# Performance work log

Measured on AMD Instinct MI355X. Metric: run time of the kernel, lower is better.

## Reference

```python
import jax, jax.numpy as jnp
import numpy as np
import heapq
from collections import defaultdict

N_PER, N_BATCH, C = 100000, 2, 128  # nodes per graph, num graphs, feature dim
TARGET = 50000                      # target node count per graph


def _build_graph():
    # Symmetric degree-4 ring graph per batch (offsets +/-1, +/-2), required so
    # neighbours[] lookups in the collapse algorithm never miss.
    within = np.tile(np.arange(N_PER), N_BATCH)
    base = np.repeat(np.arange(N_BATCH) * N_PER, N_PER)
    src_all, dst_all = [], []
    for o in (1, 2, -1, -2):
        src_all.append(base + within)
        dst_all.append(base + (within + o) % N_PER)
    ei = np.stack([np.concatenate(src_all), np.concatenate(dst_all)]).astype(np.int64)
    batch = np.repeat(np.arange(N_BATCH), N_PER).astype(np.int64)
    return ei, batch


def _collapse(x, edge_index, target_edge_count, batch):
    # Faithful port of the sequential heap-driven greedy collapse.
    N = x.shape[0]
    collapse_mask = np.ones(N, dtype=bool)
    x_mask = np.ones(N, dtype=bool)
    neighbours = defaultdict(list)
    for f, t in zip(edge_index[0].tolist(), edge_index[1].tolist()):
        neighbours[f].append(t)
    for batch_id in range(int(batch.max()) + 1):
        node_ids = np.nonzero(batch == batch_id)[0]
        num_nodes = int(node_ids.shape[0])
        mags = (x[node_ids] * x[node_ids]).sum(axis=1)  # squared magnitude priority
        heap = [[float(m), int(n)] for m, n in zip(mags, node_ids)]
        heapq.heapify(heap)
        while num_nodes > target_edge_count:
            if len(heap) == 0:
                break
            _, node_id = heapq.heappop(heap)
            node_id = int(node_id)
            if not collapse_mask[node_id]:
                continue
            collapse_mask[node_id] = False
            neighbour_ids = neighbours[node_id]
            num_nodes -= 1
            new_neighbour_ids = []
            for nb in neighbour_ids:
                x_mask[nb] = False
                collapse_mask[nb] = False
                num_nodes -= 1
                for nbnb in neighbours[nb]:
                    if nbnb in neighbour_ids or nbnb == node_id:
                        continue
                    new_neighbour_ids.append(nbnb)
                    neighbours[nbnb] = [n for n in neighbours[nbnb] if n != nb]
                    neighbours[nbnb].append(node_id)
            neighbours[node_id] = new_neighbour_ids
    # Remap surviving nodes to compact ids and rebuild edge_index.
    old_to_new = -np.ones(N, dtype=np.int64)
    new_to_old = np.nonzero(x_mask)[0]
    old_to_new[new_to_old] = np.arange(new_to_old.shape[0])
    rows, cols = [], []
    for new_id, old_id in enumerate(new_to_old.tolist()):
        for nid in neighbours[old_id]:
            rows.append(new_id)
            cols.append(int(old_to_new[nid]))
    new_ei = np.array([rows, cols], dtype=np.int64)
    return x_mask, new_ei


def setup_inputs() -> dict:
    key = jax.random.key(0)
    ei, batch = _build_graph()
    x = jax.random.normal(key, (N_BATCH * N_PER, C), dtype=jnp.float32)
    return {
        "x": x,
        "edge_index": jnp.asarray(ei),
        "target_edge_count": TARGET,
        "batch": jnp.asarray(batch),
        "vertices": jnp.zeros((1,), dtype=jnp.int32),
        "edges": jnp.zeros((1,), dtype=jnp.int32),
    }


def reference(x, edge_index, target_edge_count, batch, vertices, edges):
    # vertices/edges are unused by the original forward.
    x_mask, new_ei = _collapse(
        np.asarray(x), np.asarray(edge_index), int(target_edge_count), np.asarray(batch)
    )
    keep = jnp.asarray(np.nonzero(x_mask)[0])
    return x[keep], jnp.asarray(new_ei), batch[keep]
```

## Files before the change

kernel.cpp:

```cpp
#include <hip/hip_runtime.h>
#include <stdint.h>

#define N_PER   100000
#define N_TOT   200000
#define C_DIM   128
#define PAD     131072
#define NBLK    782
#define CMW     ((N_PER + 31) / 32)
#define MAXL    512

typedef unsigned long long u64;

#define WAIT_LDS() asm volatile("s_waitcnt lgkmcnt(0)" ::: "memory")
#define WAIT_ALL() asm volatile("s_waitcnt vmcnt(0) lgkmcnt(0)" ::: "memory")

__device__ __forceinline__ float mag128(const float4* __restrict__ p4) {
  float4 u = p4[0], v = p4[1];
  float r0 = __fmul_rn(u.x,u.x), r1 = __fmul_rn(u.y,u.y),
        r2 = __fmul_rn(u.z,u.z), r3 = __fmul_rn(u.w,u.w),
        r4 = __fmul_rn(v.x,v.x), r5 = __fmul_rn(v.y,v.y),
        r6 = __fmul_rn(v.z,v.z), r7 = __fmul_rn(v.w,v.w);
  #pragma unroll
  for (int m = 1; m < 16; ++m) {
    u = p4[2*m]; v = p4[2*m+1];
    r0 = __fadd_rn(r0, __fmul_rn(u.x,u.x));
    r1 = __fadd_rn(r1, __fmul_rn(u.y,u.y));
    r2 = __fadd_rn(r2, __fmul_rn(u.z,u.z));
    r3 = __fadd_rn(r3, __fmul_rn(u.w,u.w));
    r4 = __fadd_rn(r4, __fmul_rn(v.x,v.x));
    r5 = __fadd_rn(r5, __fmul_rn(v.y,v.y));
    r6 = __fadd_rn(r6, __fmul_rn(v.z,v.z));
    r7 = __fadd_rn(r7, __fmul_rn(v.w,v.w));
  }
  return __fadd_rn(__fadd_rn(__fadd_rn(r0,r1), __fadd_rn(r2,r3)),
                   __fadd_rn(__fadd_rn(r4,r5), __fadd_rn(r6,r7)));
}

__global__ void k_init_keys(const float* __restrict__ x, u64* __restrict__ keys) {
  int slot = blockIdx.x*blockDim.x + threadIdx.x;
  if (slot >= 2*PAD) return;
  int b = slot >> 17;
  int w = slot & (PAD-1);
  if (w < N_PER) {
    int node = b*N_PER + w;
    float mag = mag128((const float4*)(x + (size_t)node*C_DIM));
    keys[slot] = ((u64)__float_as_uint(mag) << 32) | (uint32_t)node;
  } else {
    keys[slot] = ~0ull;
  }
}

__global__ void k_init_graph(int* __restrict__ nbr, uint8_t* __restrict__ xm, int cap) {
  int node = blockIdx.x*blockDim.x + threadIdx.x;
  if (node >= N_TOT) return;
  int base = (node >= N_PER) ? N_PER : 0;
  int w = node - base;
  int* Lp = nbr + (size_t)node*cap;
  Lp[0] = 4;
  Lp[1] = base + (w + 1) % N_PER;
  Lp[2] = base + (w + 2) % N_PER;
  Lp[3] = base + (w + N_PER - 1) % N_PER;
  Lp[4] = base + (w + N_PER - 2) % N_PER;
  xm[node] = 1;
}

__global__ void k_bitonic(u64* __restrict__ keys, int k, int j) {
  int i = blockIdx.x*blockDim.x + threadIdx.x;
  if (i >= 2*PAD) return;
  int ixj = i ^ j;
  if (ixj <= i) return;
  int wi = i & (PAD-1);
  bool asc = ((wi & k) == 0);
  u64 a = keys[i], b = keys[ixj];
  bool sw = asc ? (a > b) : (a < b);
  if (sw) { keys[i] = b; keys[ixj] = a; }
}

__global__ __launch_bounds__(64) void k_collapse(const u64* __restrict__ keys,
                                                 int* __restrict__ nbr,
                                                 uint8_t* __restrict__ xm,
                                                 const int* __restrict__ tgt_p,
                                                 int cap) {
  __shared__ uint32_t s_cm[CMW];
  __shared__ uint32_t s_mm[CMW];
  __shared__ uint32_t s_dirty[CMW];
  __shared__ int      s_prow[MAXL];
  __shared__ int      s_mem[4][MAXL];
  __shared__ int      s_memlen[4];
  __shared__ int      s_cand[MAXL];

  const int b    = blockIdx.x;
  const int lane = threadIdx.x;
  const int TGT  = tgt_p[0];
  const u64* ord = keys + (size_t)b * PAD;
  const int gbase = b * N_PER;

  for (int w = lane; w < CMW; w += 64) { s_cm[w]=0xffffffffu; s_mm[w]=0u; s_dirty[w]=0u; }
  WAIT_LDS();

  int num_nodes = N_PER;
  int  pfnode = -1;
  bool pfbad  = true;
  int4 pfreg  = make_int4(0,0,0,0);

  auto drain = [&]() {
    WAIT_ALL();
    for (int w = lane; w < CMW; w += 64) s_dirty[w] = 0u;
    pfbad = true;
    WAIT_LDS();
  };

  for (int base2 = 0; base2 < N_PER && num_nodes > TGT; base2 += 64) {
    int nd_l = (base2 + lane < N_PER) ? (int)(uint32_t)ord[base2 + lane] : -1;
    bool alive = false;
    if (base2 + lane < N_PER) {
      int ll = nd_l - gbase;
      alive = ((s_cm[ll>>5] >> (ll&31)) & 1u) != 0u;
    }
    u64 mask = __ballot(alive);
    while (mask != 0ull && num_nodes > TGT) {
      int k2 = __ffsll((long long)mask) - 1;
      mask &= mask - 1ull;
      int node = __shfl(nd_l, k2);
      int local = node - gbase;
      if (((s_cm[local>>5] >> (local&31)) & 1u) == 0u) continue;

      bool ndirty = ((s_dirty[local>>5] >> (local&31)) & 1u) != 0u;
      bool usepf = (node == pfnode) && !pfbad && !ndirty;
      int4 rv = make_int4(0,0,0,0);
      if (usepf) {
        if (lane < 16) rv = pfreg;
      } else {
        if (ndirty) drain();
        if (lane < 16) rv = *(const int4*)(nbr + (size_t)node*cap + 4*lane);
      }
      int L = __shfl(rv.x, 0);
      if (lane < 16) {
        int bs = 4*lane;
        if (lane == 0) { s_prow[0]=rv.y; s_prow[1]=rv.z; s_prow[2]=rv.w; }
        else { s_prow[bs-1]=rv.x; s_prow[bs]=rv.y; s_prow[bs+1]=rv.z; s_prow[bs+2]=rv.w; }
      }
      if (L > 62) {
        for (int i = 63 + lane; i < L; i += 64) s_prow[i] = nbr[(size_t)node*cap + 1 + i];
      }
      WAIT_LDS();

      if (lane == 0) atomicAnd(&s_cm[local>>5], ~(1u << (local&31)));
      for (int i = lane; i < L; i += 64) {
        int mv = s_prow[i];
        xm[mv] = 0;
        int ml = mv - gbase;
        atomicAnd(&s_cm[ml>>5], ~(1u << (ml&31)));
        atomicOr (&s_mm[ml>>5],  1u << (ml&31));
      }
      num_nodes -= 1 + L;
      WAIT_LDS();

      {
        u64 nm = mask;
        int npf = -1;
        while (nm != 0ull) {
          int kk = __ffsll((long long)nm) - 1;
          int cnd = __shfl(nd_l, kk);
          int cl = cnd - gbase;
          if (((s_cm[cl>>5] >> (cl&31)) & 1u) != 0u) { npf = cnd; break; }
          nm &= nm - 1ull;
        }
        pfnode = npf;
        pfbad = true;
        if (npf >= 0) {
          int pl = npf - gbase;
          bool pd = ((s_dirty[pl>>5] >> (pl&31)) & 1u) != 0u;
          if (!pd) {
            pfbad = false;
            if (lane < 16) pfreg = *(const int4*)(nbr + (size_t)npf*cap + 4*lane);
          }
        }
      }

      {
        bool md = false;
        for (int i = lane; i < L; i += 64) {
          int ml = s_prow[i] - gbase;
          md |= ((s_dirty[ml>>5] >> (ml&31)) & 1u) != 0u;
        }
        if (__ballot(md) != 0ull) drain();
      }

      int Ctot = 0;
      for (int mc = 0; mc < L; mc += 4) {
        int Lc = (L - mc < 4) ? (L - mc) : 4;
        int m0 = s_prow[mc];
        int m1 = (Lc > 1) ? s_prow[mc+1] : -1;
        int m2 = (Lc > 2) ? s_prow[mc+2] : -1;
        int m3 = (Lc > 3) ? s_prow[mc+3] : -1;

        int g = lane >> 4, jj = lane & 15;
        const int* tlg = nullptr;
        if (g < Lc) {
          int m = (g==0)?m0:(g==1)?m1:(g==2)?m2:m3;
          tlg = nbr + (size_t)m * cap;
          int4 c0 = *(const int4*)(tlg + 4*jj);
          if (jj == 0) s_memlen[g] = c0.x;
          else         s_mem[g][4*jj-1] = c0.x;
          s_mem[g][4*jj+0] = c0.y;
          s_mem[g][4*jj+1] = c0.z;
          s_mem[g][4*jj+2] = c0.w;
        }
        WAIT_LDS();
        if (g < Lc) {
          int lg = s_memlen[g];
          for (int s0 = 64 + 4*jj; s0 <= lg; s0 += 64) {
            int4 cv = *(const int4*)(tlg + s0);
            s_mem[g][s0-1] = cv.x;
            if (s0+1 <= lg) s_mem[g][s0+0] = cv.y;
            if (s0+2 <= lg) s_mem[g][s0+1] = cv.z;
            if (s0+3 <= lg) s_mem[g][s0+2] = cv.w;
          }
        }
        WAIT_LDS();

        int len0=(Lc>0)?s_memlen[0]:0, len1=(Lc>1)?s_memlen[1]:0,
            len2=(Lc>2)?s_memlen[2]:0, len3=(Lc>3)?s_memlen[3]:0;
        int o1=len0, o2=o1+len1, o3=o2+len2, T=o3+len3;

        for (int cb = 0; cb < T; cb += 64) {
          int i = cb + lane;
          bool act = i < T;
          int val = -1, gg = 0;
          if (act) {
            gg = (i>=o1) + (i>=o2) + (i>=o3);
            int qb = (gg==0)?0:(gg==1)?o1:(gg==2)?o2:o3;
            val = s_mem[gg][i-qb];
          }
          bool ism = !act || (val == node);
          if (act && !ism) {
            int vl = val - gbase;
            ism |= ((s_mm[vl>>5] >> (vl&31)) & 1u) != 0u;
          }
          bool keep = act && !ism;
          u64 mk = __ballot(keep);
          int wcnt = __popcll(mk);
          if (keep) {
            int pos = Ctot + __popcll(mk & ((1ull<<lane)-1ull));
            if (pos < cap - 1) s_cand[pos] = val;
          }
          if (wcnt) {
            bool td = false;
            if (keep) {
              int vl = val - gbase;
              td = ((s_dirty[vl>>5] >> (vl&31)) & 1u) != 0u;
            }
            if (__ballot(td) != 0ull) drain();

            int Twin = (T - cb < 64) ? (T - cb) : 64;
            uint32_t pk = keep ? (((uint32_t)val << 2) | (uint32_t)gg) : 0xffffffffu;
            bool owner = keep;
            uint32_t rmg = 0;
            int kocc = 0;
            for (int q = 0; q < Twin; ++q) {
              uint32_t pq = __shfl(pk, q);
              if (pq != 0xffffffffu && keep && (int)(pq >> 2) == val) {
                rmg |= 1u << (pq & 3u);
                ++kocc;
                if (q < lane) owner = false;
              }
            }
            if (owner) {
              bool u0=(rmg&1u)!=0, u1=(rmg&2u)!=0, u2=(rmg&4u)!=0, u3=(rmg&8u)!=0;
              int* tl = nbr + (size_t)val * cap;
              int4 v0 = *(const int4*)tl;
              int4 v1 = *(const int4*)(tl + 4);
              int L3 = v0.x;
              int wslot = 1;
              if (L3 >= 1) { int e=v0.y; if (!((u0&&e==m0)||(u1&&e==m1)||(u2&&e==m2)||(u3&&e==m3))) tl[wslot++]=e; }
              if (L3 >= 2) { int e=v0.z; if (!((u0&&e==m0)||(u1&&e==m1)||(u2&&e==m2)||(u3&&e==m3))) tl[wslot++]=e; }
              if (L3 >= 3) { int e=v0.w; if (!((u0&&e==m0)||(u1&&e==m1)||(u2&&e==m2)||(u3&&e==m3))) tl[wslot++]=e; }
              if (L3 >= 4) { int e=v1.x; if (!((u0&&e==m0)||(u1&&e==m1)||(u2&&e==m2)||(u3&&e==m3))) tl[wslot++]=e; }
              if (L3 >= 5) { int e=v1.y; if (!((u0&&e==m0)||(u1&&e==m1)||(u2&&e==m2)||(u3&&e==m3))) tl[wslot++]=e; }
              if (L3 >= 6) { int e=v1.z; if (!((u0&&e==m0)||(u1&&e==m1)||(u2&&e==m2)||(u3&&e==m3))) tl[wslot++]=e; }
              if (L3 >= 7) { int e=v1.w; if (!((u0&&e==m0)||(u1&&e==m1)||(u2&&e==m2)||(u3&&e==m3))) tl[wslot++]=e; }
              for (int s0 = 8; s0 <= L3; s0 += 4) {
                int4 v = *(const int4*)(tl + s0);
                { int e=v.x; if (!((u0&&e==m0)||(u1&&e==m1)||(u2&&e==m2)||(u3&&e==m3))) tl[wslot++]=e; }
                if (s0+1 <= L3) { int e=v.y; if (!((u0&&e==m0)||(u1&&e==m1)||(u2&&e==m2)||(u3&&e==m3))) tl[wslot++]=e; }
                if (s0+2 <= L3) { int e=v.z; if (!((u0&&e==m0)||(u1&&e==m1)||(u2&&e==m2)||(u3&&e==m3))) tl[wslot++]=e; }
                if (s0+3 <= L3) { int e=v.w; if (!((u0&&e==m0)||(u1&&e==m1)||(u2&&e==m2)||(u3&&e==m3))) tl[wslot++]=e; }
              }
              int fin = wslot - 1 + kocc;
              if (fin > cap - 1) fin = cap - 1;
              for (int a = wslot; a <= fin; ++a) tl[a] = node;
              tl[0] = fin;
              int vl = val - gbase;
              atomicOr(&s_dirty[vl>>5], 1u << (vl&31));
            }
            WAIT_LDS();
          }
          Ctot += wcnt;
        }
      }

      for (int i = lane; i < L; i += 64) {
        int ml = s_prow[i] - gbase;
        atomicAnd(&s_mm[ml>>5], ~(1u << (ml&31)));
      }
      int wl = (Ctot < cap - 1) ? Ctot : (cap - 1);
      int* nodeL = nbr + (size_t)node * cap;
      if (lane == 0) {
        nodeL[0] = wl;
        atomicOr(&s_dirty[local>>5], 1u << (local&31));
      }
      for (int k3 = lane; k3 < wl; k3 += 64) nodeL[1 + k3] = s_cand[k3];
      WAIT_LDS();
    }
  }
}

__device__ __forceinline__ u64 pack_node(const uint8_t* xm, const int* nbr, int i, int cap) {
  int keep = xm[i];
  int el = keep ? nbr[(size_t)i*cap] : 0;
  return ((u64)(uint32_t)el << 32) | (uint32_t)keep;
}

__global__ void k_scan1(const uint8_t* __restrict__ xm, const int* __restrict__ nbr,
                        u64* __restrict__ bsum, int cap) {
  __shared__ u64 s[256];
  int t = threadIdx.x;
  int i = blockIdx.x*256 + t;
  u64 v = (i < N_TOT) ? pack_node(xm, nbr, i, cap) : 0ull;
  s[t] = v; __syncthreads();
  for (int off = 128; off > 0; off >>= 1) {
    if (t < off) s[t] += s[t+off];
    __syncthreads();
  }
  if (t == 0) bsum[blockIdx.x] = s[0];
}

__global__ void k_scan2(u64* __restrict__ bsum, int* __restrict__ cnt) {
  __shared__ u64 s[1024];
  int t = threadIdx.x;
  u64 v = (t < NBLK) ? bsum[t] : 0ull;
  s[t] = v; __syncthreads();
  for (int off = 1; off < 1024; off <<= 1) {
    u64 a = (t >= off) ? s[t-off] : 0ull;
    __syncthreads();
    s[t] += a;
    __syncthreads();
  }
  if (t < NBLK) bsum[t] = s[t] - v;
  if (t == 1023) {
    cnt[0] = (int)(s[1023] & 0xffffffffull);
    cnt[1] = (int)(s[1023] >> 32);
  }
}

__global__ void k_scan3(const uint8_t* __restrict__ xm, const int* __restrict__ nbr,
                        const u64* __restrict__ bsum,
                        int* __restrict__ newid, int* __restrict__ eoff, int cap) {
  __shared__ u64 s[256];
  int t = threadIdx.x;
  int i = blockIdx.x*256 + t;
  u64 v = (i < N_TOT) ? pack_node(xm, nbr, i, cap) : 0ull;
  s[t] = v; __syncthreads();
  for (int off = 1; off < 256; off <<= 1) {
    u64 a = (t >= off) ? s[t-off] : 0ull;
    __syncthreads();
    s[t] += a;
    __syncthreads();
  }
  u64 excl = s[t] - v + bsum[blockIdx.x];
  if (i < N_TOT) {
    newid[i] = (int)(excl & 0xffffffffull);
    eoff[i]  = (int)(excl >> 32);
  }
}

__global__ void k_write_x(const float* __restrict__ x, const uint8_t* __restrict__ xm,
                          const int* __restrict__ newid, float* __restrict__ out) {
  int tid = blockIdx.x*blockDim.x + threadIdx.x;
  int node = tid >> 5, q = tid & 31;
  if (node >= N_TOT || !xm[node]) return;
  const float4* src = (const float4*)(x + (size_t)node*C_DIM);
  float4* dst = (float4*)(out + (size_t)newid[node]*C_DIM);
  dst[q] = src[q];
}

__global__ __launch_bounds__(64) void k_write_edges(const uint8_t* __restrict__ xm,
                              const int* __restrict__ nbr,
                              const int* __restrict__ newid, const int* __restrict__ eoff,
                              const int* __restrict__ cnt, float* __restrict__ out, int cap) {
  int node = blockIdx.x;
  int lane = threadIdx.x;
  if (!xm[node]) return;
  int K = cnt[0], E = cnt[1];
  size_t base = (size_t)K * C_DIM;
  int nid = newid[node];
  if (lane == 0) out[base + 2*(size_t)E + nid] = (node >= N_PER) ? 1.0f : 0.0f;
  int len = nbr[(size_t)node*cap];
  int eo = eoff[node];
  for (int j = lane; j < len; j += 64) {
    int ent = nbr[(size_t)node*cap + 1 + j];
    int off = eo + j;
    out[base + off]             = (float)nid;
    out[base + (size_t)E + off] = xm[ent] ? (float)newid[ent] : -1.0f;
  }
}

extern "C" void kernel_launch(void* const* d_in, const int* in_sizes, int n_in,
                              void* d_out, int out_size, void* d_ws, size_t ws_size,
                              hipStream_t stream) {
  const float* x   = (const float*)d_in[0];
  const int*   tgt = (const int*)d_in[2];
  float* out = (float*)d_out;
  uint8_t* ws = (uint8_t*)d_ws;

  size_t off = 0;
  auto alloc = [&](size_t bytes) -> void* {
    void* p = ws + off;
    off += (bytes + 255) & ~(size_t)255;
    return p;
  };
  u64*     keys  = (u64*)alloc((size_t)2*PAD*8);
  uint8_t* xm    = (uint8_t*)alloc(N_TOT);
  int*     newid = (int*)alloc((size_t)N_TOT*4);
  int*     eoff  = (int*)alloc((size_t)N_TOT*4);
  u64*     bsum  = (u64*)alloc((size_t)1024*8);
  int*     cnt   = (int*)alloc(256);
  size_t remain = (ws_size > off + 64) ? (ws_size - off - 64) : 0;
  int cap = (int)(remain / ((size_t)N_TOT * 4));
  cap &= ~3;
  if (cap > 512) cap = 512;
  if (cap < 68)  cap = 68;
  int* nbr = (int*)(ws + off);

  k_init_keys<<<(2*PAD)/256, 256, 0, stream>>>(x, keys);
  k_init_graph<<<NBLK, 256, 0, stream>>>(nbr, xm, cap);

  for (int k = 2; k <= PAD; k <<= 1)
    for (int j = k >> 1; j >= 1; j >>= 1)
      k_bitonic<<<(2*PAD)/256, 256, 0, stream>>>(keys, k, j);

  k_collapse<<<2, 64, 0, stream>>>(keys, nbr, xm, tgt, cap);

  k_scan1<<<NBLK, 256, 0, stream>>>(xm, nbr, bsum, cap);
  k_scan2<<<1, 1024, 0, stream>>>(bsum, cnt);
  k_scan3<<<NBLK, 256, 0, stream>>>(xm, nbr, bsum, newid, eoff, cap);

  k_write_x<<<(N_TOT*32)/256, 256, 0, stream>>>(x, xm, newid, out);
  k_write_edges<<<N_TOT, 64, 0, stream>>>(xm, nbr, newid, eoff, cnt, out, cap);
}
```

Baseline: 45.38 ms.

## Process 16 neighbour rows per batch in collapse step instead of 4

Widens the neighbour-row gather in the sequential collapse loop from 4 rows per batch to 16, with 4 lanes per row for the first 16 entries and a second pass for longer rows. Prefix offsets go into shared memory. Target-list head loads are now issued by every kept lane before the duplicate-detection shuffle loop, so their latency overlaps with it. It also invalidates the prefetched next node when it is touched. The aim is fewer serial iterations and better latency hiding in a latency-bound single-wave loop, at the cost of more LDS, a full 64-step shuffle loop and a 16-way removal test per element.

```diff
diff --git a/kernel.cpp b/kernel.cpp
--- a/kernel.cpp
+++ b/kernel.cpp
@@ -85,8 +85,9 @@
   __shared__ uint32_t s_mm[CMW];
   __shared__ uint32_t s_dirty[CMW];
   __shared__ int      s_prow[MAXL];
-  __shared__ int      s_mem[4][MAXL];
-  __shared__ int      s_memlen[4];
+  __shared__ int      s_mem[16][MAXL];
+  __shared__ int      s_memlen[16];
+  __shared__ int      s_off[17];
   __shared__ int      s_cand[MAXL];
 
   const int b    = blockIdx.x;
@@ -188,50 +189,85 @@
       }
 
       int Ctot = 0;
-      for (int mc = 0; mc < L; mc += 4) {
-        int Lc = (L - mc < 4) ? (L - mc) : 4;
-        int m0 = s_prow[mc];
-        int m1 = (Lc > 1) ? s_prow[mc+1] : -1;
-        int m2 = (Lc > 2) ? s_prow[mc+2] : -1;
-        int m3 = (Lc > 3) ? s_prow[mc+3] : -1;
-
-        int g = lane >> 4, jj = lane & 15;
-        const int* tlg = nullptr;
-        if (g < Lc) {
-          int m = (g==0)?m0:(g==1)?m1:(g==2)?m2:m3;
-          tlg = nbr + (size_t)m * cap;
-          int4 c0 = *(const int4*)(tlg + 4*jj);
-          if (jj == 0) s_memlen[g] = c0.x;
-          else         s_mem[g][4*jj-1] = c0.x;
-          s_mem[g][4*jj+0] = c0.y;
-          s_mem[g][4*jj+1] = c0.z;
-          s_mem[g][4*jj+2] = c0.w;
+      for (int gb = 0; gb < L; gb += 16) {
+        int G = (L - gb < 16) ? (L - gb) : 16;
+
+        int r = lane >> 2, q4 = lane & 3;
+        if (r < G) {
+          int m = s_prow[gb + r];
+          const int* tlg = nbr + (size_t)m * cap;
+          int4 c0 = *(const int4*)(tlg + 4*q4);
+          if (q4 == 0) s_memlen[r] = c0.x;
+          else         s_mem[r][4*q4-1] = c0.x;
+          s_mem[r][4*q4+0] = c0.y;
+          s_mem[r][4*q4+1] = c0.z;
+          s_mem[r][4*q4+2] = c0.w;
         }
         WAIT_LDS();
-        if (g < Lc) {
-          int lg = s_memlen[g];
-          for (int s0 = 64 + 4*jj; s0 <= lg; s0 += 64) {
-            int4 cv = *(const int4*)(tlg + s0);
-            s_mem[g][s0-1] = cv.x;
-            if (s0+1 <= lg) s_mem[g][s0+0] = cv.y;
-            if (s0+2 <= lg) s_mem[g][s0+1] = cv.z;
-            if (s0+3 <= lg) s_mem[g][s0+2] = cv.w;
-          }
+        {
+          int tr = lane >> 4, tq = lane & 15;
+          for (int br = 0; br < G; br += 4) {
+            int rr = br + tr;
+            bool ok = (rr < G) && (s_memlen[rr] > 15);
+            if (__ballot(ok) == 0ull) continue;
+            if (ok) {
+              int m = s_prow[gb + rr];
+              const int* t2 = nbr + (size_t)m * cap;
+              int len = s_memlen[rr];
+              for (int s0 = 16 + 4*tq; s0 <= len; s0 += 64) {
+                int4 cv = *(const int4*)(t2 + s0);
+                s_mem[rr][s0-1] = cv.x;
+                if (s0+1 <= len) s_mem[rr][s0+0] = cv.y;
+                if (s0+2 <= len) s_mem[rr][s0+1] = cv.z;
+                if (s0+3 <= len) s_mem[rr][s0+2] = cv.w;
+              }
+            }
+          }
+          WAIT_LDS();
+        }
+
+        if (lane == 0) {
+          int a = 0; s_off[0] = 0;
+          for (int k3 = 0; k3 < 16; ++k3) { a += (k3 < G) ? s_memlen[k3] : 0; s_off[k3+1] = a; }
         }
         WAIT_LDS();
-
-        int len0=(Lc>0)?s_memlen[0]:0, len1=(Lc>1)?s_memlen[1]:0,
-            len2=(Lc>2)?s_memlen[2]:0, len3=(Lc>3)?s_memlen[3]:0;
-        int o1=len0, o2=o1+len1, o3=o2+len2, T=o3+len3;
+        int o1=s_off[1], o2=s_off[2], o3=s_off[3], o4=s_off[4], o5=s_off[5],
+            o6=s_off[6], o7=s_off[7], o8=s_off[8], o9=s_off[9], o10=s_off[10],
+            o11=s_off[11], o12=s_off[12], o13=s_off[13], o14=s_off[14], o15=s_off[15];
+        int T = s_off[16];
+        int mv0 =(G>0)? s_prow[gb+0]:-1, mv1 =(G>1)? s_prow[gb+1]:-1,
+            mv2 =(G>2)? s_prow[gb+2]:-1, mv3 =(G>3)? s_prow[gb+3]:-1,
+            mv4 =(G>4)? s_prow[gb+4]:-1, mv5 =(G>5)? s_prow[gb+5]:-1,
+            mv6 =(G>6)? s_prow[gb+6]:-1, mv7 =(G>7)? s_prow[gb+7]:-1,
+            mv8 =(G>8)? s_prow[gb+8]:-1, mv9 =(G>9)? s_prow[gb+9]:-1,
+            mv10=(G>10)?s_prow[gb+10]:-1, mv11=(G>11)?s_prow[gb+11]:-1,
+            mv12=(G>12)?s_prow[gb+12]:-1, mv13=(G>13)?s_prow[gb+13]:-1,
+            mv14=(G>14)?s_prow[gb+14]:-1, mv15=(G>15)?s_prow[gb+15]:-1;
+        WAIT_LDS();
+
+        auto rmtest = [&](uint32_t rmg, int e) -> bool {
+          return ((rmg&0x0001u)&&e==mv0 )||((rmg&0x0002u)&&e==mv1 )||
+                 ((rmg&0x0004u)&&e==mv2 )||((rmg&0x0008u)&&e==mv3 )||
+                 ((rmg&0x0010u)&&e==mv4 )||((rmg&0x0020u)&&e==mv5 )||
+                 ((rmg&0x0040u)&&e==mv6 )||((rmg&0x0080u)&&e==mv7 )||
+                 ((rmg&0x0100u)&&e==mv8 )||((rmg&0x0200u)&&e==mv9 )||
+                 ((rmg&0x0400u)&&e==mv10)||((rmg&0x0800u)&&e==mv11)||
+                 ((rmg&0x1000u)&&e==mv12)||((rmg&0x2000u)&&e==mv13)||
+                 ((rmg&0x4000u)&&e==mv14)||((rmg&0x8000u)&&e==mv15);
+        };
 
         for (int cb = 0; cb < T; cb += 64) {
           int i = cb + lane;
           bool act = i < T;
-          int val = -1, gg = 0;
+          int gg = 0, val = -1;
           if (act) {
-            gg = (i>=o1) + (i>=o2) + (i>=o3);
-            int qb = (gg==0)?0:(gg==1)?o1:(gg==2)?o2:o3;
-            val = s_mem[gg][i-qb];
+            gg = (i>=o1)+(i>=o2)+(i>=o3)+(i>=o4)+(i>=o5)+(i>=o6)+(i>=o7)+(i>=o8)
+               + (i>=o9)+(i>=o10)+(i>=o11)+(i>=o12)+(i>=o13)+(i>=o14)+(i>=o15);
+            int st = (gg==0)?0:(gg==1)?o1:(gg==2)?o2:(gg==3)?o3:(gg==4)?o4:
+                     (gg==5)?o5:(gg==6)?o6:(gg==7)?o7:(gg==8)?o8:(gg==9)?o9:
+                     (gg==10)?o10:(gg==11)?o11:(gg==12)?o12:(gg==13)?o13:
+                     (gg==14)?o14:o15;
+            val = s_mem[gg][i - st];
           }
           bool ism = !act || (val == node);
           if (act && !ism) {
@@ -246,6 +282,7 @@
             if (pos < cap - 1) s_cand[pos] = val;
           }
           if (wcnt) {
+            if (!pfbad && (__ballot(keep && (val == pfnode)) != 0ull)) pfbad = true;
             bool td = false;
             if (keep) {
               int vl = val - gbase;
@@ -253,43 +290,46 @@
             }
             if (__ballot(td) != 0ull) drain();
 
-            int Twin = (T - cb < 64) ? (T - cb) : 64;
-            uint32_t pk = keep ? (((uint32_t)val << 2) | (uint32_t)gg) : 0xffffffffu;
+            int* tl = nullptr;
+            int4 v0 = make_int4(0,0,0,0), v1 = make_int4(0,0,0,0);
+            if (keep) {
+              tl = nbr + (size_t)val * cap;
+              v0 = *(const int4*)tl;
+              v1 = *(const int4*)(tl + 4);
+            }
+
+            uint32_t pk_ = keep ? (((uint32_t)val << 4) | (uint32_t)gg) : 0xffffffffu;
             bool owner = keep;
             uint32_t rmg = 0;
             int kocc = 0;
-            for (int q = 0; q < Twin; ++q) {
-              uint32_t pq = __shfl(pk, q);
-              if (pq != 0xffffffffu && keep && (int)(pq >> 2) == val) {
-                rmg |= 1u << (pq & 3u);
+            for (int q = 0; q < 64; ++q) {
+              uint32_t pq = __shfl(pk_, q);
+              if (pq != 0xffffffffu && keep && (int)(pq >> 4) == val) {
+                rmg |= 1u << (pq & 15u);
                 ++kocc;
                 if (q < lane) owner = false;
               }
             }
             if (owner) {
-              bool u0=(rmg&1u)!=0, u1=(rmg&2u)!=0, u2=(rmg&4u)!=0, u3=(rmg&8u)!=0;
-              int* tl = nbr + (size_t)val * cap;
-              int4 v0 = *(const int4*)tl;
-              int4 v1 = *(const int4*)(tl + 4);
               int L3 = v0.x;
               int wslot = 1;
-              if (L3 >= 1) { int e=v0.y; if (!((u0&&e==m0)||(u1&&e==m1)||(u2&&e==m2)||(u3&&e==m3))) tl[wslot++]=e; }
-              if (L3 >= 2) { int e=v0.z; if (!((u0&&e==m0)||(u1&&e==m1)||(u2&&e==m2)||(u3&&e==m3))) tl[wslot++]=e; }
-              if (L3 >= 3) { int e=v0.w; if (!((u0&&e==m0)||(u1&&e==m1)||(u2&&e==m2)||(u3&&e==m3))) tl[wslot++]=e; }
-              if (L3 >= 4) { int e=v1.x; if (!((u0&&e==m0)||(u1&&e==m1)||(u2&&e==m2)||(u3&&e==m3))) tl[wslot++]=e; }
-              if (L3 >= 5) { int e=v1.y; if (!((u0&&e==m0)||(u1&&e==m1)||(u2&&e==m2)||(u3&&e==m3))) tl[wslot++]=e; }
-              if (L3 >= 6) { int e=v1.z; if (!((u0&&e==m0)||(u1&&e==m1)||(u2&&e==m2)||(u3&&e==m3))) tl[wslot++]=e; }
-              if (L3 >= 7) { int e=v1.w; if (!((u0&&e==m0)||(u1&&e==m1)||(u2&&e==m2)||(u3&&e==m3))) tl[wslot++]=e; }
+              if (L3 >= 1) { int e=v0.y; if (!rmtest(rmg,e)) tl[wslot++]=e; }
+              if (L3 >= 2) { int e=v0.z; if (!rmtest(rmg,e)) tl[wslot++]=e; }
+              if (L3 >= 3) { int e=v0.w; if (!rmtest(rmg,e)) tl[wslot++]=e; }
+              if (L3 >= 4) { int e=v1.x; if (!rmtest(rmg,e)) tl[wslot++]=e; }
+              if (L3 >= 5) { int e=v1.y; if (!rmtest(rmg,e)) tl[wslot++]=e; }
+              if (L3 >= 6) { int e=v1.z; if (!rmtest(rmg,e)) tl[wslot++]=e; }
+              if (L3 >= 7) { int e=v1.w; if (!rmtest(rmg,e)) tl[wslot++]=e; }
               for (int s0 = 8; s0 <= L3; s0 += 4) {
                 int4 v = *(const int4*)(tl + s0);
-                { int e=v.x; if (!((u0&&e==m0)||(u1&&e==m1)||(u2&&e==m2)||(u3&&e==m3))) tl[wslot++]=e; }
-                if (s0+1 <= L3) { int e=v.y; if (!((u0&&e==m0)||(u1&&e==m1)||(u2&&e==m2)||(u3&&e==m3))) tl[wslot++]=e; }
-                if (s0+2 <= L3) { int e=v.z; if (!((u0&&e==m0)||(u1&&e==m1)||(u2&&e==m2)||(u3&&e==m3))) tl[wslot++]=e; }
-                if (s0+3 <= L3) { int e=v.w; if (!((u0&&e==m0)||(u1&&e==m1)||(u2&&e==m2)||(u3&&e==m3))) tl[wslot++]=e; }
+                { int e=v.x; if (!rmtest(rmg,e)) tl[wslot++]=e; }
+                if (s0+1 <= L3) { int e=v.y; if (!rmtest(rmg,e)) tl[wslot++]=e; }
+                if (s0+2 <= L3) { int e=v.z; if (!rmtest(rmg,e)) tl[wslot++]=e; }
+                if (s0+3 <= L3) { int e=v.w; if (!rmtest(rmg,e)) tl[wslot++]=e; }
               }
               int fin = wslot - 1 + kocc;
               if (fin > cap - 1) fin = cap - 1;
-              for (int a = wslot; a <= fin; ++a) tl[a] = node;
+              for (int a2 = wslot; a2 <= fin; ++a2) tl[a2] = node;
               tl[0] = fin;
               int vl = val - gbase;
               atomicOr(&s_dirty[vl>>5], 1u << (vl&31));
```

Result: slower. 99.68 ms (+119.7%).
